# Kernel tuning notes

Hardware: AMD Instinct MI355X
Metric: run time of the kernel (lower is better)

The kernel has to match this reference:

```python
import jax, jax.numpy as jnp
import numpy as np

N_EMBD = 1024
N_HEAD = 16
HEAD_DIM = N_EMBD // N_HEAD  # 64
N_CTX = 2048
ROPE_THETA = 10000.0


def _rope_cache(L, dim, base):
    inv_freq = 1.0 / (base ** (np.arange(0, dim, 2, dtype=np.float32) / dim))
    t = np.arange(L, dtype=np.float32)
    freqs = np.einsum('i,j->ij', t, inv_freq)  # (L, dim/2)
    return jnp.asarray(np.cos(freqs)), jnp.asarray(np.sin(freqs))


def _apply_rotary(x, cos, sin):
    # x: (B, H, L, D), cos/sin: (L, D/2) -> broadcast (1,1,L,D/2)
    x1 = x[..., ::2]
    x2 = x[..., 1::2]
    c = cos[None, None, :, :]
    s = sin[None, None, :, :]
    y1 = x1 * c - x2 * s
    y2 = x1 * s + x2 * c
    # interleave back: stack on last dim then flatten
    return jnp.stack((y1, y2), axis=-1).reshape(x.shape)


def setup_inputs() -> dict:
    key = jax.random.key(0)
    k1, k2, k3, k4, k5 = jax.random.split(key, 5)
    B, L, D = 4, 2048, N_EMBD
    scale = 0.02
    x = jax.random.normal(k1, (B, L, D), dtype=jnp.float32)
    W_qkv = jax.random.normal(k2, (D, 3 * D), dtype=jnp.float32) * scale
    b_qkv = jnp.zeros((3 * D,), dtype=jnp.float32)
    W_proj = jax.random.normal(k3, (D, D), dtype=jnp.float32) * scale
    b_proj = jnp.zeros((D,), dtype=jnp.float32)
    attention_mask = jnp.ones((B, L), dtype=jnp.int32)
    return {"x": x, "W_qkv": W_qkv, "b_qkv": b_qkv, "W_proj": W_proj,
            "b_proj": b_proj, "attention_mask": attention_mask}


def reference(x, W_qkv, b_qkv, W_proj, b_proj, attention_mask):
    B, L, D = x.shape
    H, Dh = N_HEAD, HEAD_DIM
    qkv = x @ W_qkv + b_qkv  # (B, L, 3D)
    q, k, v = jnp.split(qkv, 3, axis=2)
    # (B, L, H, Dh) -> (B, H, L, Dh)
    q = q.reshape(B, L, H, Dh).transpose(0, 2, 1, 3)
    k = k.reshape(B, L, H, Dh).transpose(0, 2, 1, 3)
    v = v.reshape(B, L, H, Dh).transpose(0, 2, 1, 3)
    cos, sin = _rope_cache(L, Dh, ROPE_THETA)
    q = _apply_rotary(q, cos, sin)
    k = _apply_rotary(k, cos, sin)
    # mask: causal & key padding keep
    causal = jnp.tril(jnp.ones((L, L), dtype=bool))[None, None]        # (1,1,L,L)
    key_keep = attention_mask.astype(bool)[:, None, None, :]          # (B,1,1,L)
    keep = causal & key_keep                                          # (B,1,L,L)
    scores = jnp.einsum('bhqd,bhkd->bhqk', q, k) / jnp.sqrt(jnp.float32(Dh))
    scores = jnp.where(keep, scores, jnp.finfo(scores.dtype).min)
    attn = jax.nn.softmax(scores, axis=-1)
    out = jnp.einsum('bhqk,bhkd->bhqd', attn, v)  # (B,H,L,Dh)
    out = out.transpose(0, 2, 1, 3).reshape(B, L, D)
    return out @ W_proj + b_proj
```

## Files before the change

kernel.cpp:

```cpp
#include <hip/hip_runtime.h>
#include <math.h>

typedef __bf16 bf16x8 __attribute__((ext_vector_type(8)));
typedef float f32x4 __attribute__((ext_vector_type(4)));
typedef float f32x16 __attribute__((ext_vector_type(16)));
typedef unsigned short u16;
typedef unsigned short u16x8 __attribute__((ext_vector_type(8)));
typedef unsigned short u16x4 __attribute__((ext_vector_type(4)));
typedef unsigned u32x2v __attribute__((ext_vector_type(2)));

#define BATCH 4
#define SEQ   2048
#define EMBD  1024
#define NHEAD 16
#define HDIM  64
#define MROWS 8192
#define QKVN  3072

__device__ __forceinline__ u16 f2bf(float f) {
    union { float f; unsigned u; } cv; cv.f = f;
    unsigned u = cv.u;
    return (u16)((u + 0x7FFFu + ((u >> 16) & 1u)) >> 16);
}

__device__ __forceinline__ unsigned cvtpk_bf16(float lo, float hi) {
    unsigned r;
    asm("v_cvt_pk_bf16_f32 %0, %1, %2" : "=v"(r) : "v"(lo), "v"(hi));
    return r;
}

__device__ __forceinline__ void glds16(const void* g, void* l) {
    __builtin_amdgcn_global_load_lds(
        (const __attribute__((address_space(1))) unsigned int*)(g),
        (__attribute__((address_space(3))) unsigned int*)(l), 16, 0, 0);
}

#define MF8(qm, A0, A1, A2, A3, B0, B1)                                          \
    acc[(qm)*4+0][0] = __builtin_amdgcn_mfma_f32_16x16x32_bf16(A0, B0, acc[(qm)*4+0][0], 0, 0, 0); \
    acc[(qm)*4+0][1] = __builtin_amdgcn_mfma_f32_16x16x32_bf16(A0, B1, acc[(qm)*4+0][1], 0, 0, 0); \
    acc[(qm)*4+1][0] = __builtin_amdgcn_mfma_f32_16x16x32_bf16(A1, B0, acc[(qm)*4+1][0], 0, 0, 0); \
    acc[(qm)*4+1][1] = __builtin_amdgcn_mfma_f32_16x16x32_bf16(A1, B1, acc[(qm)*4+1][1], 0, 0, 0); \
    acc[(qm)*4+2][0] = __builtin_amdgcn_mfma_f32_16x16x32_bf16(A2, B0, acc[(qm)*4+2][0], 0, 0, 0); \
    acc[(qm)*4+2][1] = __builtin_amdgcn_mfma_f32_16x16x32_bf16(A2, B1, acc[(qm)*4+2][1], 0, 0, 0); \
    acc[(qm)*4+3][0] = __builtin_amdgcn_mfma_f32_16x16x32_bf16(A3, B0, acc[(qm)*4+3][0], 0, 0, 0); \
    acc[(qm)*4+3][1] = __builtin_amdgcn_mfma_f32_16x16x32_bf16(A3, B1, acc[(qm)*4+3][1], 0, 0, 0);

__device__ __forceinline__ void transpose_body(const float* __restrict__ W,
                                               u16* __restrict__ Wt, int K, int N,
                                               int n0, int k0, u16 (*T)[68]) {
    const int tx = threadIdx.x & 15, ty = threadIdx.x >> 4;
#pragma unroll
    for (int r = 0; r < 4; r++) {
        int k = k0 + ty + r * 16;
        float4 w = *(const float4*)&W[(size_t)k * N + n0 + tx * 4];
        T[tx * 4 + 0][ty + r * 16] = f2bf(w.x);
        T[tx * 4 + 1][ty + r * 16] = f2bf(w.y);
        T[tx * 4 + 2][ty + r * 16] = f2bf(w.z);
        T[tx * 4 + 3][ty + r * 16] = f2bf(w.w);
    }
    __syncthreads();
#pragma unroll
    for (int r = 0; r < 4; r++) {
        int nl = ty + r * 16;
        u16x4 v = { T[nl][tx * 4 + 0], T[nl][tx * 4 + 1],
                    T[nl][tx * 4 + 2], T[nl][tx * 4 + 3] };
        *(u16x4*)&Wt[(size_t)(n0 + nl) * K + k0 + tx * 4] = v;
    }
}

__global__ __launch_bounds__(256)
void prep_kernel(const float* __restrict__ x, const float* __restrict__ Wqkv,
                 const float* __restrict__ Wproj, const int* __restrict__ amask,
                 u16* __restrict__ Xb, u16* __restrict__ Wqkvt, u16* __restrict__ Wprojt,
                 float* __restrict__ ropeC, float* __restrict__ ropeS,
                 float* __restrict__ mbias, int* __restrict__ flags) {
    __shared__ union { u16 T[64][68]; int ok[4]; } sm;
    const int bx = blockIdx.x, tid = threadIdx.x;
    if (bx < 8192) {
        int i = bx * 256 + tid;
        float4 v = ((const float4*)x)[i];
        u16x4 o = { f2bf(v.x), f2bf(v.y), f2bf(v.z), f2bf(v.w) };
        ((u16x4*)Xb)[i] = o;
    } else if (bx < 8960) {
        int bxx = bx - 8192;
        transpose_body(Wqkv, Wqkvt, EMBD, QKVN, (bxx % 48) * 64, (bxx / 48) * 64, sm.T);
    } else if (bx < 9216) {
        int bxx = bx - 8960;
        transpose_body(Wproj, Wprojt, EMBD, EMBD, (bxx & 15) * 64, (bxx >> 4) * 64, sm.T);
    } else if (bx < 9472) {
        int i = (bx - 9216) * 256 + tid;
        int l = i >> 5, p = i & 31;
        float invf = powf(10000.0f, -(float)(2 * p) * (1.0f / 64.0f));
        float sv, cv;
        sincosf((float)l * invf, &sv, &cv);
        ropeC[i] = cv; ropeS[i] = sv;
    } else {
        int idx = (bx - 9472) * 256 + tid;
        int mv = amask[idx];
        mbias[idx] = mv ? 0.0f : -1e30f;
        unsigned long long bal = __ballot(mv != 0);
        int wv = tid >> 6;
        if ((tid & 63) == 0) sm.ok[wv] = (bal == 0xFFFFFFFFFFFFFFFFull);
        __syncthreads();
        if (tid == 0)   flags[idx >> 7] = sm.ok[0] & sm.ok[1];
        if (tid == 128) flags[idx >> 7] = sm.ok[2] & sm.ok[3];
    }
}

__global__ __launch_bounds__(512, 2)
void qkv_gemm(const u16* __restrict__ A, const u16* __restrict__ Bt,
              const float* __restrict__ bias,
              const float* __restrict__ Ct, const float* __restrict__ St,
              u16* __restrict__ Qo, u16* __restrict__ Ko, u16* __restrict__ Vt) {
    __shared__ u16 SM[49152];
    const int tid = threadIdx.x;
    const int w = tid >> 6, ln = tid & 63;
    const int quad = ln >> 4, l16 = ln & 15;
    const int wm = w >> 2, wn = w & 3;
    const int bid = blockIdx.y * 24 + blockIdx.x;
    const int swz = (bid & 7) * 96 + (bid >> 3);
    const int m0 = (swz / 24) * 256, n0 = (swz % 24) * 128;

    const int sr8 = ln >> 3;
    const int xs = (ln & 7) ^ sr8;
    const u16* Ab = A  + (size_t)(m0 + w * 8 + sr8) * EMBD + xs * 8;
    const u16* Bb = Bt + (size_t)(n0 + w * 8 + sr8) * EMBD + xs * 8;
    u16* ldsA = SM + w * 512;
    u16* ldsB = SM + 32768 + w * 512;
    const int ch0 = ((0 + quad) ^ (l16 & 7)) * 8;
    const int ch1 = ((4 + quad) ^ (l16 & 7)) * 8;

    auto stageA = [&](int buf, int rb, int kt) {
        glds16(Ab + (size_t)rb * EMBD + kt * 64, ldsA + buf * 16384 + rb * 64);
    };
    auto stageB = [&](int buf, int rb, int kt) {
        glds16(Bb + (size_t)rb * EMBD + kt * 64, ldsB + buf * 8192 + rb * 64);
    };

    f32x4 acc[8][2] = {};

    stageA(0, 0, 0);  stageA(0, 128, 0);
    stageA(0, 64, 0); stageA(0, 192, 0);
    stageB(0, 0, 0);  stageB(0, 64, 0);
    stageA(1, 0, 1);  stageA(1, 128, 1);
    asm volatile("s_waitcnt vmcnt(2)" ::: "memory");
    __builtin_amdgcn_sched_barrier(0);
    __builtin_amdgcn_s_barrier();

    for (int u = 0; u < 16; ++u) {
        const int c = u & 1, nc = c ^ 1;
        const u16* Ac0 = SM + c * 16384 + (wm * 128 + l16) * 64;
        const u16* Ac1 = Ac0 + 64 * 64;
        const u16* Bc  = SM + 32768 + c * 8192 + (wn * 32 + l16) * 64;
        bf16x8 a0, a1, a2, a3, bk0a, bk0b, bk1a, bk1b;
        a0 = *(const bf16x8*)&Ac0[ch0];        a1 = *(const bf16x8*)&Ac0[1024 + ch0];
        a2 = *(const bf16x8*)&Ac0[2048 + ch0]; a3 = *(const bf16x8*)&Ac0[3072 + ch0];
        bk0a = *(const bf16x8*)&Bc[ch0];       bk0b = *(const bf16x8*)&Bc[1024 + ch0];
        if (u < 15) { stageA(nc, 64, u + 1); stageA(nc, 192, u + 1); stageB(nc, 64, u + 1); }
        __builtin_amdgcn_sched_barrier(0);
        __builtin_amdgcn_s_setprio(1);
        MF8(0, a0, a1, a2, a3, bk0a, bk0b);
        __builtin_amdgcn_s_setprio(0);
        __builtin_amdgcn_sched_barrier(0);
        a0 = *(const bf16x8*)&Ac0[ch1];        a1 = *(const bf16x8*)&Ac0[1024 + ch1];
        a2 = *(const bf16x8*)&Ac0[2048 + ch1]; a3 = *(const bf16x8*)&Ac0[3072 + ch1];
        bk1a = *(const bf16x8*)&Bc[ch1];       bk1b = *(const bf16x8*)&Bc[1024 + ch1];
        if (u < 15) stageB(nc, 0, u + 1);
        __builtin_amdgcn_sched_barrier(0);
        __builtin_amdgcn_s_setprio(1);
        MF8(0, a0, a1, a2, a3, bk1a, bk1b);
        __builtin_amdgcn_s_setprio(0);
        __builtin_amdgcn_sched_barrier(0);
        __builtin_amdgcn_s_barrier();
        a0 = *(const bf16x8*)&Ac1[ch0];        a1 = *(const bf16x8*)&Ac1[1024 + ch0];
        a2 = *(const bf16x8*)&Ac1[2048 + ch0]; a3 = *(const bf16x8*)&Ac1[3072 + ch0];
        if (u < 14) { stageA(c, 0, u + 2); stageA(c, 128, u + 2); }
        __builtin_amdgcn_sched_barrier(0);
        __builtin_amdgcn_s_setprio(1);
        MF8(1, a0, a1, a2, a3, bk0a, bk0b);
        __builtin_amdgcn_s_setprio(0);
        __builtin_amdgcn_sched_barrier(0);
        a0 = *(const bf16x8*)&Ac1[ch1];        a1 = *(const bf16x8*)&Ac1[1024 + ch1];
        a2 = *(const bf16x8*)&Ac1[2048 + ch1]; a3 = *(const bf16x8*)&Ac1[3072 + ch1];
        __builtin_amdgcn_sched_barrier(0);
        __builtin_amdgcn_s_setprio(1);
        MF8(1, a0, a1, a2, a3, bk1a, bk1b);
        __builtin_amdgcn_s_setprio(0);
        __builtin_amdgcn_sched_barrier(0);
        if (u < 14) asm volatile("s_waitcnt vmcnt(2)" ::: "memory");
        else        asm volatile("s_waitcnt vmcnt(0)" ::: "memory");
        __builtin_amdgcn_sched_barrier(0);
        __builtin_amdgcn_s_barrier();
    }

    const int sec = n0 >> 10;
    if (sec == 2) {
        u16* Vl = SM;
#pragma unroll
        for (int ii = 0; ii < 8; ii++)
#pragma unroll
            for (int j = 0; j < 2; j++) {
                int nl = wn * 32 + j * 16 + l16;
                int ml = wm * 128 + ii * 16 + quad * 4;
                int n = n0 + wn * 32 + j * 16 + l16;
                u16x4 pk;
#pragma unroll
                for (int r = 0; r < 4; r++)
                    pk[r] = f2bf(acc[ii][j][r] + bias[n]);
                *(u16x4*)&Vl[nl * 260 + ml] = pk;
            }
        __syncthreads();
        {
            int dcl = tid >> 2, ck = tid & 3;
            int dcol = (n0 & 1023) + dcl;
            int h = dcol >> 6, dh = dcol & 63;
            int b = m0 >> 11, l0 = m0 & 2047;
            size_t gb = (((size_t)b * NHEAD + h) * HDIM + dh) * SEQ + l0 + ck * 64;
#pragma unroll
            for (int c2 = 0; c2 < 8; c2++) {
                u16x8 v = *(const u16x8*)&Vl[dcl * 260 + ck * 64 + c2 * 8];
                *(u16x8*)&Vt[gb + c2 * 8] = v;
            }
        }
    } else {
        u16* O = (sec == 0) ? Qo : Ko;
        const float qs = (sec == 0) ? 0.125f * 1.44269504f : 1.0f;
#pragma unroll
        for (int ii = 0; ii < 8; ii++)
#pragma unroll
            for (int r = 0; r < 4; r++) {
                int m = m0 + wm * 128 + ii * 16 + quad * 4 + r;
                int b = m >> 11, l = m & 2047;
#pragma unroll
                for (int j = 0; j < 2; j++) {
                    int n = n0 + wn * 32 + j * 16 + l16;
                    int h = (n & 1023) >> 6, dh = n & 63;
                    int p = (n & 63) >> 1;
                    float v = acc[ii][j][r] + bias[n];
                    float pv = __shfl_xor(v, 1, 64);
                    float cv = Ct[l * 32 + p], sv = St[l * 32 + p];
                    float o = (l16 & 1) ? (pv * sv + v * cv) : (v * cv - pv * sv);
                    O[(((size_t)b * NHEAD + h) * SEQ + l) * HDIM + dh] = f2bf(o * qs);
                }
            }
    }
}

__global__ __launch_bounds__(512, 2)
void attn_mfma3(const u16* __restrict__ Qb, const u16* __restrict__ Kb,
                const u16* __restrict__ Vt, const float* __restrict__ mb,
                const int* __restrict__ flags, u16* __restrict__ Ot) {
    __shared__ u16 SM[32768];
    const int tid = threadIdx.x;
    const int wv = tid >> 6, ln = tid & 63;
    const int l32 = ln & 31, hi = ln >> 5;
    const int bid = blockIdx.x;
    const int bh = bid & 63;
    const int qt = (bid < 256) ? 7 - (bid >> 6) : ((bid - 256) >> 6);
    const int b = bh >> 4;
    const u16* Qg = Qb + (size_t)bh * SEQ * HDIM;
    const u16* Kg = Kb + (size_t)bh * SEQ * HDIM;
    const u16* Vg = Vt + (size_t)bh * HDIM * SEQ;

    const int kRow = ln >> 3;
    const size_t kLane = (size_t)(wv * 16 + kRow) * 64 + ((ln & 7) ^ kRow) * 8;
    const int vRow = ln >> 4, sc0 = (ln & 15) ^ vRow;
    const size_t vLaneE = (size_t)(wv * 8 + vRow) * SEQ + sc0 * 8;
    const size_t vLaneO = (size_t)(wv * 8 + 4 + vRow) * SEQ + (sc0 ^ 4) * 8;

    const int q0w = qt * 256 + wv * 32;
    const int qabs = q0w + l32;

    bf16x8 Qf[4];
#pragma unroll
    for (int kd = 0; kd < 4; kd++)
        Qf[kd] = *(const bf16x8*)&Qg[(size_t)(q0w + l32) * HDIM + kd * 16 + hi * 8];

    f32x16 o[2] = {};
    float mrun = -1e30f, lrun = 0.f;

    const int nkt = 2 * qt + 2;

    {
        u16* KsD = SM + wv * 1024;
        u16* VsD = SM + 8192 + wv * 1024;
        glds16(Kg + kLane,       KsD);
        glds16(Kg + kLane + 512, KsD + 512);
        glds16(Vg + vLaneE,      VsD);
        glds16(Vg + vLaneO,      VsD + 512);
    }
    __syncthreads();

    int buf = 0;
    for (int kt = 0; kt < nkt; kt++) {
        const int kbase = kt * 128;
        if (kt + 1 < nkt) {
            const size_t nb = (size_t)(kbase + 128);
            u16* KsD = SM + (buf ^ 1) * 16384 + wv * 1024;
            u16* VsD = SM + (buf ^ 1) * 16384 + 8192 + wv * 1024;
            glds16(Kg + nb * 64 + kLane,       KsD);
            glds16(Kg + nb * 64 + kLane + 512, KsD + 512);
            glds16(Vg + nb + vLaneE,           VsD);
            glds16(Vg + nb + vLaneO,           VsD + 512);
        }
        const u16* Ks = SM + buf * 16384;
        const u16* Vs = SM + buf * 16384 + 8192;

        if (kbase <= q0w + 31) {
            f32x16 s[4];
            __builtin_amdgcn_s_setprio(1);
#pragma unroll
            for (int mi = 0; mi < 4; mi++) {
                const int key = mi * 32 + l32;
                f32x16 z = {};
#pragma unroll
                for (int kd = 0; kd < 4; kd++) {
                    int ch = kd * 2 + hi;
                    bf16x8 kf = *(const bf16x8*)&Ks[key * 64 + ((ch ^ (key & 7)) * 8)];
                    z = __builtin_amdgcn_mfma_f32_32x32x16_bf16(kf, Qf[kd], z, 0, 0, 0);
                }
                s[mi] = z;
            }
            __builtin_amdgcn_s_setprio(0);

            if (kbase + 127 > q0w) {
#pragma unroll
                for (int mi = 0; mi < 4; mi++)
#pragma unroll
                    for (int r = 0; r < 16; r++) {
                        int row = kbase + mi * 32 + (r & 3) + 8 * (r >> 2) + 4 * hi;
                        if (row > qabs) s[mi][r] = -1e30f;
                    }
            }
            if (!flags[b * 16 + kt]) {
#pragma unroll
                for (int mi = 0; mi < 4; mi++)
#pragma unroll
                    for (int r = 0; r < 16; r++) {
                        int row = mi * 32 + (r & 3) + 8 * (r >> 2) + 4 * hi;
                        s[mi][r] += mb[b * SEQ + kbase + row];
                    }
            }

            float rm = -1e30f;
#pragma unroll
            for (int mi = 0; mi < 4; mi++) {
                float a0 = fmaxf(fmaxf(s[mi][0],  s[mi][1]),  fmaxf(s[mi][2],  s[mi][3]));
                float a1 = fmaxf(fmaxf(s[mi][4],  s[mi][5]),  fmaxf(s[mi][6],  s[mi][7]));
                float a2 = fmaxf(fmaxf(s[mi][8],  s[mi][9]),  fmaxf(s[mi][10], s[mi][11]));
                float a3 = fmaxf(fmaxf(s[mi][12], s[mi][13]), fmaxf(s[mi][14], s[mi][15]));
                rm = fmaxf(rm, fmaxf(fmaxf(a0, a1), fmaxf(a2, a3)));
            }
            {
                u32x2v f = __builtin_amdgcn_permlane32_swap(
                    __float_as_uint(rm), __float_as_uint(rm), false, false);
                rm = fmaxf(__uint_as_float(f[0]), __uint_as_float(f[1]));
            }
            if (!__all(rm <= mrun + 8.0f)) {
                float mnew = fmaxf(mrun, rm);
                float al = __builtin_amdgcn_exp2f(mrun - mnew);
                mrun = mnew;
                lrun *= al;
#pragma unroll
                for (int r = 0; r < 16; r++) { o[0][r] *= al; o[1][r] *= al; }
            }
            float rs = 0.f;
#pragma unroll
            for (int mi = 0; mi < 4; mi++) {
                float ps = 0.f;
#pragma unroll
                for (int r = 0; r < 16; r++) {
                    float pe = __builtin_amdgcn_exp2f(s[mi][r] - mrun);
                    s[mi][r] = pe;
                    ps += pe;
                }
                rs += ps;
            }
            {
                u32x2v f = __builtin_amdgcn_permlane32_swap(
                    __float_as_uint(rs), __float_as_uint(rs), false, false);
                rs = __uint_as_float(f[0]) + __uint_as_float(f[1]);
            }
            lrun += rs;

#pragma unroll
            for (int t = 0; t < 4; t++) {
                unsigned A0 = cvtpk_bf16(s[t][0],  s[t][1]);
                unsigned B0 = cvtpk_bf16(s[t][4],  s[t][5]);
                unsigned A1 = cvtpk_bf16(s[t][2],  s[t][3]);
                unsigned B1 = cvtpk_bf16(s[t][6],  s[t][7]);
                u32x2v r0 = __builtin_amdgcn_permlane32_swap(A0, B0, false, false);
                u32x2v r1 = __builtin_amdgcn_permlane32_swap(A1, B1, false, false);
                union { unsigned u[4]; bf16x8 v; } p0;
                p0.u[0] = r0[0]; p0.u[1] = r1[0]; p0.u[2] = r0[1]; p0.u[3] = r1[1];

                unsigned A2 = cvtpk_bf16(s[t][8],  s[t][9]);
                unsigned B2 = cvtpk_bf16(s[t][12], s[t][13]);
                unsigned A3 = cvtpk_bf16(s[t][10], s[t][11]);
                unsigned B3 = cvtpk_bf16(s[t][14], s[t][15]);
                u32x2v r2 = __builtin_amdgcn_permlane32_swap(A2, B2, false, false);
                u32x2v r3 = __builtin_amdgcn_permlane32_swap(A3, B3, false, false);
                union { unsigned u[4]; bf16x8 v; } p1;
                p1.u[0] = r2[0]; p1.u[1] = r3[0]; p1.u[2] = r2[1]; p1.u[3] = r3[1];

                __builtin_amdgcn_s_setprio(1);
#pragma unroll
                for (int md = 0; md < 2; md++) {
                    const int dh = md * 32 + l32;
                    bf16x8 v0 = *(const bf16x8*)&Vs[dh * 128 + (((t * 4 + hi)     ^ (dh & 7)) * 8)];
                    o[md] = __builtin_amdgcn_mfma_f32_32x32x16_bf16(v0, p0.v, o[md], 0, 0, 0);
                    bf16x8 v1 = *(const bf16x8*)&Vs[dh * 128 + (((t * 4 + 2 + hi) ^ (dh & 7)) * 8)];
                    o[md] = __builtin_amdgcn_mfma_f32_32x32x16_bf16(v1, p1.v, o[md], 0, 0, 0);
                }
                __builtin_amdgcn_s_setprio(0);
            }
        }
        __syncthreads();
        buf ^= 1;
    }

    __syncthreads();
    u16* Osh = SM + wv * 2176;
    float inv = 1.0f / lrun;
#pragma unroll
    for (int md = 0; md < 2; md++)
#pragma unroll
        for (int r = 0; r < 16; r++) {
            int dh = md * 32 + (r & 3) + 8 * (r >> 2) + 4 * hi;
            Osh[l32 * 68 + dh] = f2bf(o[md][r] * inv);
        }
    __syncthreads();
    {
        int qrow = ln >> 1, hf = ln & 1;
        size_t gbase = ((size_t)bh * SEQ + q0w + qrow) * HDIM + hf * 32;
#pragma unroll
        for (int c = 0; c < 4; c++) {
            u16x8 vv = *(const u16x8*)&Osh[qrow * 68 + hf * 32 + c * 8];
            *(u16x8*)&Ot[gbase + c * 8] = vv;
        }
    }
}

__global__ __launch_bounds__(256)
void proj_gemm(const u16* __restrict__ A, const u16* __restrict__ Bt,
               const float* __restrict__ bias, float* __restrict__ out) {
    __shared__ u16 SM[32768];
    const int tid = threadIdx.x;
    const int wv = tid >> 6, ln = tid & 63;
    const int quad = ln >> 4, l16 = ln & 15;
    const int bid = blockIdx.y * 8 + blockIdx.x;
    const int swz = (bid & 7) * 64 + (bid >> 3);
    const int m0 = (swz >> 3) * 128, n0 = (swz & 7) * 128;
    const int wm = wv >> 1, wn = wv & 1;

    const int srow = wv * 8 + (ln >> 3);
    const int xs = (ln & 7) ^ (srow & 7);

    f32x4 acc[4][4] = {};

    auto stage = [&](int buf, int kt) {
        u16* As = SM + buf * 16384;
        u16* Bs = As + 8192;
#pragma unroll
        for (int p = 0; p < 4; p++) {
            int row = p * 32 + srow;
            int m = m0 + row;
            int bb = m >> 11, l = m & 2047;
            glds16(A + (((size_t)(bb * 16 + kt) * SEQ + l) * HDIM) + xs * 8,
                   As + (p * 256 + wv * 64) * 8);
            glds16(Bt + (size_t)(n0 + row) * EMBD + kt * 64 + xs * 8,
                   Bs + (p * 256 + wv * 64) * 8);
        }
    };

    stage(0, 0);
    __syncthreads();
    int buf = 0;
    for (int kt = 0; kt < 16; kt++) {
        if (kt < 15) stage(buf ^ 1, kt + 1);
        const u16* As = SM + buf * 16384;
        const u16* Bs = As + 8192;
        __builtin_amdgcn_s_setprio(1);
#pragma unroll
        for (int kk = 0; kk < 2; kk++) {
            bf16x8 af[4], bfr[4];
#pragma unroll
            for (int i = 0; i < 4; i++) {
                int R = wm * 64 + i * 16 + l16;
                af[i] = *(const bf16x8*)&As[R * 64 + (((kk * 4 + quad) ^ (R & 7)) * 8)];
            }
#pragma unroll
            for (int j = 0; j < 4; j++) {
                int R = wn * 64 + j * 16 + l16;
                bfr[j] = *(const bf16x8*)&Bs[R * 64 + (((kk * 4 + quad) ^ (R & 7)) * 8)];
            }
#pragma unroll
            for (int i = 0; i < 4; i++)
#pragma unroll
                for (int j = 0; j < 4; j++)
                    acc[i][j] = __builtin_amdgcn_mfma_f32_16x16x32_bf16(af[i], bfr[j], acc[i][j], 0, 0, 0);
        }
        __builtin_amdgcn_s_setprio(0);
        __syncthreads();
        buf ^= 1;
    }
#pragma unroll
    for (int i = 0; i < 4; i++)
#pragma unroll
        for (int r = 0; r < 4; r++) {
            int m = m0 + wm * 64 + i * 16 + quad * 4 + r;
#pragma unroll
            for (int j = 0; j < 4; j++) {
                int n = n0 + wn * 64 + j * 16 + l16;
                out[(size_t)m * EMBD + n] = acc[i][j][r] + bias[n];
            }
        }
}

extern "C" void kernel_launch(void* const* d_in, const int* in_sizes, int n_in,
                              void* d_out, int out_size, void* d_ws, size_t ws_size,
                              hipStream_t stream)
{
    const float* x     = (const float*)d_in[0];
    const float* Wqkv  = (const float*)d_in[1];
    const float* bqkv  = (const float*)d_in[2];
    const float* Wproj = (const float*)d_in[3];
    const float* bproj = (const float*)d_in[4];
    const int*   amask = (const int*)d_in[5];
    float* out = (float*)d_out;

    char* ws = (char*)d_ws;
    u16*   Xb     = (u16*)(ws);
    u16*   Ot     = (u16*)(ws);
    u16*   Wqkvt  = (u16*)(ws + 16777216);
    u16*   Wprojt = (u16*)(ws + 23068672);
    u16*   Qb     = (u16*)(ws + 25165824);
    u16*   Kb     = (u16*)(ws + 41943040);
    u16*   Vtp    = (u16*)(ws + 75497472);
    float* ropeC  = (float*)(ws + 92274688);
    float* ropeS  = (float*)(ws + 92536832);
    float* mbias  = (float*)(ws + 92798976);
    int*   flags  = (int*)(ws + 92831744);

    prep_kernel<<<9504, 256, 0, stream>>>(x, Wqkv, Wproj, amask,
                                          Xb, Wqkvt, Wprojt, ropeC, ropeS, mbias, flags);
    qkv_gemm<<<dim3(24, 32), 512, 0, stream>>>(
        Xb, Wqkvt, bqkv, ropeC, ropeS, Qb, Kb, Vtp);
    attn_mfma3<<<512, 512, 0, stream>>>(Qb, Kb, Vtp, mbias, flags, Ot);
    proj_gemm<<<dim3(EMBD / 128, MROWS / 128), 256, 0, stream>>>(Ot, Wprojt, bproj, out);
}
```

Before: 243.8 us.

## Halve attention block to 4 waves, each processing two query strips

The attention kernel now launches 256 threads instead of 512, and each wave handles two 32-row query strips (q0 and q0+128) against the same shared K/V tile. Each wave loads twice as much of the K/V tile into shared memory, and output staging covers both strips. The aim is to reuse K/V fragments across strips with fewer waves and barriers. The cost is roughly doubled register state per wave (two Q sets and two accumulators), which may lower occupancy, and causal work becomes less balanced across the two strips.

Result: slower. 292.0 us (+19.8%).

```diff
diff --git a/kernel.cpp b/kernel.cpp
--- a/kernel.cpp
+++ b/kernel.cpp
@@ -246,7 +246,7 @@
     }
 }
 
-__global__ __launch_bounds__(512, 2)
+__global__ __launch_bounds__(256)
 void attn_mfma3(const u16* __restrict__ Qb, const u16* __restrict__ Kb,
                 const u16* __restrict__ Vt, const float* __restrict__ mb,
                 const int* __restrict__ flags, u16* __restrict__ Ot) {
@@ -263,31 +263,146 @@
     const u16* Vg = Vt + (size_t)bh * HDIM * SEQ;
 
     const int kRow = ln >> 3;
-    const size_t kLane = (size_t)(wv * 16 + kRow) * 64 + ((ln & 7) ^ kRow) * 8;
+    const size_t kLane = (size_t)(wv * 32 + kRow) * 64 + ((ln & 7) ^ kRow) * 8;
     const int vRow = ln >> 4, sc0 = (ln & 15) ^ vRow;
-    const size_t vLaneE = (size_t)(wv * 8 + vRow) * SEQ + sc0 * 8;
-    const size_t vLaneO = (size_t)(wv * 8 + 4 + vRow) * SEQ + (sc0 ^ 4) * 8;
-
-    const int q0w = qt * 256 + wv * 32;
-    const int qabs = q0w + l32;
-
-    bf16x8 Qf[4];
-#pragma unroll
-    for (int kd = 0; kd < 4; kd++)
-        Qf[kd] = *(const bf16x8*)&Qg[(size_t)(q0w + l32) * HDIM + kd * 16 + hi * 8];
-
-    f32x16 o[2] = {};
-    float mrun = -1e30f, lrun = 0.f;
+    const size_t vLaneE = (size_t)(wv * 16 + vRow) * SEQ + sc0 * 8;
+    const size_t vLaneO = (size_t)(wv * 16 + vRow) * SEQ + (sc0 ^ 4) * 8;
+
+    const int q0a = qt * 256 + wv * 32;
+    const int q0b = q0a + 128;
+
+    bf16x8 Qfa[4], Qfb[4];
+#pragma unroll
+    for (int kd = 0; kd < 4; kd++) {
+        Qfa[kd] = *(const bf16x8*)&Qg[(size_t)(q0a + l32) * HDIM + kd * 16 + hi * 8];
+        Qfb[kd] = *(const bf16x8*)&Qg[(size_t)(q0b + l32) * HDIM + kd * 16 + hi * 8];
+    }
+
+    f32x16 oa[2] = {}, ob[2] = {};
+    float ma = -1e30f, la = 0.f, mbr = -1e30f, lb = 0.f;
 
     const int nkt = 2 * qt + 2;
 
+    auto strip = [&](const bf16x8* Qf, f32x16* o, float& mrun, float& lrun,
+                     int q0, const u16* Ks, const u16* Vs, int kbase, int kt) {
+        f32x16 s[4];
+        __builtin_amdgcn_s_setprio(1);
+#pragma unroll
+        for (int mi = 0; mi < 4; mi++) {
+            const int key = mi * 32 + l32;
+            f32x16 z = {};
+#pragma unroll
+            for (int kd = 0; kd < 4; kd++) {
+                int ch = kd * 2 + hi;
+                bf16x8 kf = *(const bf16x8*)&Ks[key * 64 + ((ch ^ (key & 7)) * 8)];
+                z = __builtin_amdgcn_mfma_f32_32x32x16_bf16(kf, Qf[kd], z, 0, 0, 0);
+            }
+            s[mi] = z;
+        }
+        __builtin_amdgcn_s_setprio(0);
+
+        if (kbase + 127 > q0) {
+            const int qabs = q0 + l32;
+#pragma unroll
+            for (int mi = 0; mi < 4; mi++)
+#pragma unroll
+                for (int r = 0; r < 16; r++) {
+                    int row = kbase + mi * 32 + (r & 3) + 8 * (r >> 2) + 4 * hi;
+                    if (row > qabs) s[mi][r] = -1e30f;
+                }
+        }
+        if (!flags[b * 16 + kt]) {
+#pragma unroll
+            for (int mi = 0; mi < 4; mi++)
+#pragma unroll
+                for (int r = 0; r < 16; r++) {
+                    int row = mi * 32 + (r & 3) + 8 * (r >> 2) + 4 * hi;
+                    s[mi][r] += mb[b * SEQ + kbase + row];
+                }
+        }
+
+        float rm = -1e30f;
+#pragma unroll
+        for (int mi = 0; mi < 4; mi++) {
+            float a0 = fmaxf(fmaxf(s[mi][0],  s[mi][1]),  fmaxf(s[mi][2],  s[mi][3]));
+            float a1 = fmaxf(fmaxf(s[mi][4],  s[mi][5]),  fmaxf(s[mi][6],  s[mi][7]));
+            float a2 = fmaxf(fmaxf(s[mi][8],  s[mi][9]),  fmaxf(s[mi][10], s[mi][11]));
+            float a3 = fmaxf(fmaxf(s[mi][12], s[mi][13]), fmaxf(s[mi][14], s[mi][15]));
+            rm = fmaxf(rm, fmaxf(fmaxf(a0, a1), fmaxf(a2, a3)));
+        }
+        {
+            u32x2v f = __builtin_amdgcn_permlane32_swap(
+                __float_as_uint(rm), __float_as_uint(rm), false, false);
+            rm = fmaxf(__uint_as_float(f[0]), __uint_as_float(f[1]));
+        }
+        if (!__all(rm <= mrun + 8.0f)) {
+            float mnew = fmaxf(mrun, rm);
+            float al = __builtin_amdgcn_exp2f(mrun - mnew);
+            mrun = mnew;
+            lrun *= al;
+#pragma unroll
+            for (int r = 0; r < 16; r++) { o[0][r] *= al; o[1][r] *= al; }
+        }
+        float rs = 0.f;
+#pragma unroll
+        for (int mi = 0; mi < 4; mi++) {
+            float ps = 0.f;
+#pragma unroll
+            for (int r = 0; r < 16; r++) {
+                float pe = __builtin_amdgcn_exp2f(s[mi][r] - mrun);
+                s[mi][r] = pe;
+                ps += pe;
+            }
+            rs += ps;
+        }
+        {
+            u32x2v f = __builtin_amdgcn_permlane32_swap(
+                __float_as_uint(rs), __float_as_uint(rs), false, false);
+            rs = __uint_as_float(f[0]) + __uint_as_float(f[1]);
+        }
+        lrun += rs;
+
+#pragma unroll
+        for (int t = 0; t < 4; t++) {
+            unsigned A0 = cvtpk_bf16(s[t][0],  s[t][1]);
+            unsigned B0 = cvtpk_bf16(s[t][4],  s[t][5]);
+            unsigned A1 = cvtpk_bf16(s[t][2],  s[t][3]);
+            unsigned B1 = cvtpk_bf16(s[t][6],  s[t][7]);
+            u32x2v r0 = __builtin_amdgcn_permlane32_swap(A0, B0, false, false);
+            u32x2v r1 = __builtin_amdgcn_permlane32_swap(A1, B1, false, false);
+            union { unsigned u[4]; bf16x8 v; } p0;
+            p0.u[0] = r0[0]; p0.u[1] = r1[0]; p0.u[2] = r0[1]; p0.u[3] = r1[1];
+
+            unsigned A2 = cvtpk_bf16(s[t][8],  s[t][9]);
+            unsigned B2 = cvtpk_bf16(s[t][12], s[t][13]);
+            unsigned A3 = cvtpk_bf16(s[t][10], s[t][11]);
+            unsigned B3 = cvtpk_bf16(s[t][14], s[t][15]);
+            u32x2v r2 = __builtin_amdgcn_permlane32_swap(A2, B2, false, false);
+            u32x2v r3 = __builtin_amdgcn_permlane32_swap(A3, B3, false, false);
+            union { unsigned u[4]; bf16x8 v; } p1;
+            p1.u[0] = r2[0]; p1.u[1] = r3[0]; p1.u[2] = r2[1]; p1.u[3] = r3[1];
+
+            __builtin_amdgcn_s_setprio(1);
+#pragma unroll
+            for (int md = 0; md < 2; md++) {
+                const int dh = md * 32 + l32;
+                bf16x8 v0 = *(const bf16x8*)&Vs[dh * 128 + (((t * 4 + hi)     ^ (dh & 7)) * 8)];
+                o[md] = __builtin_amdgcn_mfma_f32_32x32x16_bf16(v0, p0.v, o[md], 0, 0, 0);
+                bf16x8 v1 = *(const bf16x8*)&Vs[dh * 128 + (((t * 4 + 2 + hi) ^ (dh & 7)) * 8)];
+                o[md] = __builtin_amdgcn_mfma_f32_32x32x16_bf16(v1, p1.v, o[md], 0, 0, 0);
+            }
+            __builtin_amdgcn_s_setprio(0);
+        }
+    };
+
     {
-        u16* KsD = SM + wv * 1024;
-        u16* VsD = SM + 8192 + wv * 1024;
-        glds16(Kg + kLane,       KsD);
-        glds16(Kg + kLane + 512, KsD + 512);
-        glds16(Vg + vLaneE,      VsD);
-        glds16(Vg + vLaneO,      VsD + 512);
+        u16* KsD = SM + wv * 2048;
+        u16* VsD = SM + 8192 + wv * 2048;
+#pragma unroll
+        for (int p = 0; p < 4; p++) {
+            glds16(Kg + kLane + p * 512, KsD + p * 512);
+            glds16(Vg + ((p & 1) ? vLaneO : vLaneE) + (size_t)p * 4 * SEQ, VsD + p * 512);
+        }
     }
     __syncthreads();
 
@@ -296,147 +411,47 @@
         const int kbase = kt * 128;
         if (kt + 1 < nkt) {
             const size_t nb = (size_t)(kbase + 128);
-            u16* KsD = SM + (buf ^ 1) * 16384 + wv * 1024;
-            u16* VsD = SM + (buf ^ 1) * 16384 + 8192 + wv * 1024;
-            glds16(Kg + nb * 64 + kLane,       KsD);
-            glds16(Kg + nb * 64 + kLane + 512, KsD + 512);
-            glds16(Vg + nb + vLaneE,           VsD);
-            glds16(Vg + nb + vLaneO,           VsD + 512);
+            u16* KsD = SM + (buf ^ 1) * 16384 + wv * 2048;
+            u16* VsD = SM + (buf ^ 1) * 16384 + 8192 + wv * 2048;
+#pragma unroll
+            for (int p = 0; p < 4; p++) {
+                glds16(Kg + nb * 64 + kLane + p * 512, KsD + p * 512);
+                glds16(Vg + nb + ((p & 1) ? vLaneO : vLaneE) + (size_t)p * 4 * SEQ, VsD + p * 512);
+            }
         }
         const u16* Ks = SM + buf * 16384;
         const u16* Vs = SM + buf * 16384 + 8192;
 
-        if (kbase <= q0w + 31) {
-            f32x16 s[4];
-            __builtin_amdgcn_s_setprio(1);
-#pragma unroll
-            for (int mi = 0; mi < 4; mi++) {
-                const int key = mi * 32 + l32;
-                f32x16 z = {};
-#pragma unroll
-                for (int kd = 0; kd < 4; kd++) {
-                    int ch = kd * 2 + hi;
-                    bf16x8 kf = *(const bf16x8*)&Ks[key * 64 + ((ch ^ (key & 7)) * 8)];
-                    z = __builtin_amdgcn_mfma_f32_32x32x16_bf16(kf, Qf[kd], z, 0, 0, 0);
-                }
-                s[mi] = z;
-            }
-            __builtin_amdgcn_s_setprio(0);
-
-            if (kbase + 127 > q0w) {
-#pragma unroll
-                for (int mi = 0; mi < 4; mi++)
-#pragma unroll
-                    for (int r = 0; r < 16; r++) {
-                        int row = kbase + mi * 32 + (r & 3) + 8 * (r >> 2) + 4 * hi;
-                        if (row > qabs) s[mi][r] = -1e30f;
-                    }
-            }
-            if (!flags[b * 16 + kt]) {
-#pragma unroll
-                for (int mi = 0; mi < 4; mi++)
-#pragma unroll
-                    for (int r = 0; r < 16; r++) {
-                        int row = mi * 32 + (r & 3) + 8 * (r >> 2) + 4 * hi;
-                        s[mi][r] += mb[b * SEQ + kbase + row];
-                    }
-            }
-
-            float rm = -1e30f;
-#pragma unroll
-            for (int mi = 0; mi < 4; mi++) {
-                float a0 = fmaxf(fmaxf(s[mi][0],  s[mi][1]),  fmaxf(s[mi][2],  s[mi][3]));
-                float a1 = fmaxf(fmaxf(s[mi][4],  s[mi][5]),  fmaxf(s[mi][6],  s[mi][7]));
-                float a2 = fmaxf(fmaxf(s[mi][8],  s[mi][9]),  fmaxf(s[mi][10], s[mi][11]));
-                float a3 = fmaxf(fmaxf(s[mi][12], s[mi][13]), fmaxf(s[mi][14], s[mi][15]));
-                rm = fmaxf(rm, fmaxf(fmaxf(a0, a1), fmaxf(a2, a3)));
-            }
-            {
-                u32x2v f = __builtin_amdgcn_permlane32_swap(
-                    __float_as_uint(rm), __float_as_uint(rm), false, false);
-                rm = fmaxf(__uint_as_float(f[0]), __uint_as_float(f[1]));
-            }
-            if (!__all(rm <= mrun + 8.0f)) {
-                float mnew = fmaxf(mrun, rm);
-                float al = __builtin_amdgcn_exp2f(mrun - mnew);
-                mrun = mnew;
-                lrun *= al;
-#pragma unroll
-                for (int r = 0; r < 16; r++) { o[0][r] *= al; o[1][r] *= al; }
-            }
-            float rs = 0.f;
-#pragma unroll
-            for (int mi = 0; mi < 4; mi++) {
-                float ps = 0.f;
-#pragma unroll
-                for (int r = 0; r < 16; r++) {
-                    float pe = __builtin_amdgcn_exp2f(s[mi][r] - mrun);
-                    s[mi][r] = pe;
-                    ps += pe;
-                }
-                rs += ps;
-            }
-            {
-                u32x2v f = __builtin_amdgcn_permlane32_swap(
-                    __float_as_uint(rs), __float_as_uint(rs), false, false);
-                rs = __uint_as_float(f[0]) + __uint_as_float(f[1]);
-            }
-            lrun += rs;
-
-#pragma unroll
-            for (int t = 0; t < 4; t++) {
-                unsigned A0 = cvtpk_bf16(s[t][0],  s[t][1]);
-                unsigned B0 = cvtpk_bf16(s[t][4],  s[t][5]);
-                unsigned A1 = cvtpk_bf16(s[t][2],  s[t][3]);
-                unsigned B1 = cvtpk_bf16(s[t][6],  s[t][7]);
-                u32x2v r0 = __builtin_amdgcn_permlane32_swap(A0, B0, false, false);
-                u32x2v r1 = __builtin_amdgcn_permlane32_swap(A1, B1, false, false);
-                union { unsigned u[4]; bf16x8 v; } p0;
-                p0.u[0] = r0[0]; p0.u[1] = r1[0]; p0.u[2] = r0[1]; p0.u[3] = r1[1];
-
-                unsigned A2 = cvtpk_bf16(s[t][8],  s[t][9]);
-                unsigned B2 = cvtpk_bf16(s[t][12], s[t][13]);
-                unsigned A3 = cvtpk_bf16(s[t][10], s[t][11]);
-                unsigned B3 = cvtpk_bf16(s[t][14], s[t][15]);
-                u32x2v r2 = __builtin_amdgcn_permlane32_swap(A2, B2, false, false);
-                u32x2v r3 = __builtin_amdgcn_permlane32_swap(A3, B3, false, false);
-                union { unsigned u[4]; bf16x8 v; } p1;
-                p1.u[0] = r2[0]; p1.u[1] = r3[0]; p1.u[2] = r2[1]; p1.u[3] = r3[1];
-
-                __builtin_amdgcn_s_setprio(1);
-#pragma unroll
-                for (int md = 0; md < 2; md++) {
-                    const int dh = md * 32 + l32;
-                    bf16x8 v0 = *(const bf16x8*)&Vs[dh * 128 + (((t * 4 + hi)     ^ (dh & 7)) * 8)];
-                    o[md] = __builtin_amdgcn_mfma_f32_32x32x16_bf16(v0, p0.v, o[md], 0, 0, 0);
-                    bf16x8 v1 = *(const bf16x8*)&Vs[dh * 128 + (((t * 4 + 2 + hi) ^ (dh & 7)) * 8)];
-                    o[md] = __builtin_amdgcn_mfma_f32_32x32x16_bf16(v1, p1.v, o[md], 0, 0, 0);
-                }
-                __builtin_amdgcn_s_setprio(0);
-            }
-        }
+        if (kbase <= q0a + 31) strip(Qfa, oa, ma, la, q0a, Ks, Vs, kbase, kt);
+        if (kbase <= q0b + 31) strip(Qfb, ob, mbr, lb, q0b, Ks, Vs, kbase, kt);
+
         __syncthreads();
         buf ^= 1;
     }
 
     __syncthreads();
-    u16* Osh = SM + wv * 2176;
-    float inv = 1.0f / lrun;
-#pragma unroll
-    for (int md = 0; md < 2; md++)
-#pragma unroll
-        for (int r = 0; r < 16; r++) {
-            int dh = md * 32 + (r & 3) + 8 * (r >> 2) + 4 * hi;
-            Osh[l32 * 68 + dh] = f2bf(o[md][r] * inv);
-        }
-    __syncthreads();
     {
+        u16* OshA = SM + wv * 2176;
+        u16* OshB = SM + (4 + wv) * 2176;
+        float ia = 1.0f / la, ib = 1.0f / lb;
+#pragma unroll
+        for (int md = 0; md < 2; md++)
+#pragma unroll
+            for (int r = 0; r < 16; r++) {
+                int dh = md * 32 + (r & 3) + 8 * (r >> 2) + 4 * hi;
+                OshA[l32 * 68 + dh] = f2bf(oa[md][r] * ia);
+                OshB[l32 * 68 + dh] = f2bf(ob[md][r] * ib);
+            }
+        __syncthreads();
         int qrow = ln >> 1, hf = ln & 1;
-        size_t gbase = ((size_t)bh * SEQ + q0w + qrow) * HDIM + hf * 32;
+        size_t gA = ((size_t)bh * SEQ + q0a + qrow) * HDIM + hf * 32;
+        size_t gB = ((size_t)bh * SEQ + q0b + qrow) * HDIM + hf * 32;
 #pragma unroll
         for (int c = 0; c < 4; c++) {
-            u16x8 vv = *(const u16x8*)&Osh[qrow * 68 + hf * 32 + c * 8];
-            *(u16x8*)&Ot[gbase + c * 8] = vv;
+            u16x8 va = *(const u16x8*)&OshA[qrow * 68 + hf * 32 + c * 8];
+            *(u16x8*)&Ot[gA + c * 8] = va;
+            u16x8 vb = *(const u16x8*)&OshB[qrow * 68 + hf * 32 + c * 8];
+            *(u16x8*)&Ot[gB + c * 8] = vb;
         }
     }
 }
@@ -546,6 +561,6 @@
                                           Xb, Wqkvt, Wprojt, ropeC, ropeS, mbias, flags);
     qkv_gemm<<<dim3(24, 32), 512, 0, stream>>>(
         Xb, Wqkvt, bqkv, ropeC, ropeS, Qb, Kb, Vtp);
-    attn_mfma3<<<512, 512, 0, stream>>>(Qb, Kb, Vtp, mbias, flags, Ot);
+    attn_mfma3<<<512, 256, 0, stream>>>(Qb, Kb, Vtp, mbias, flags, Ot);
     proj_gemm<<<dim3(EMBD / 128, MROWS / 128), 256, 0, stream>>>(Ot, Wprojt, bproj, out);
 }
```
